# Kernel tuning notes

Measured on AMD Instinct MI355X. Metric: run time of the kernel, lower is better.

The kernel has to match this reference:

```python
import jax, jax.numpy as jnp
import numpy as np

B, N, C, K = 4, 4096, 64, 16
EPS = 1e-5


def _bn(x, g, b, m, v):
    # eval-mode BatchNorm2d on [B, C, N, K]
    scale = (g / jnp.sqrt(v + EPS))[None, :, None, None]
    return (x - m[None, :, None, None]) * scale + b[None, :, None, None]


def setup_inputs() -> dict:
    key = jax.random.key(0)
    ks = jax.random.split(key, 32)
    s = 0.05
    inp = {
        "p": jax.random.normal(ks[0], (B, N, 3), jnp.float32),
        "x": jax.random.normal(ks[1], (B, C, N), jnp.float32),
        "mask": jnp.ones((B, N), dtype=bool),
        # q/k/v 1x1 Conv1d weights [out, in] + bias
        "Wq": jax.random.normal(ks[2], (C, C)) * s, "bq": jax.random.normal(ks[3], (C,)) * s,
        "Wk": jax.random.normal(ks[4], (C, C)) * s, "bk": jax.random.normal(ks[5], (C,)) * s,
        "Wv": jax.random.normal(ks[6], (C, C)) * s, "bv": jax.random.normal(ks[7], (C,)) * s,
        # pos-enc: Conv2d(3->C, no bias), BN, ReLU, Conv2d(C->C)
        "pe_w1": jax.random.normal(ks[8], (C, 3)) * s,
        "pe_bn_g": jax.random.normal(ks[9], (C,)) * s + 1.0,
        "pe_bn_b": jax.random.normal(ks[10], (C,)) * s,
        "pe_bn_m": jax.random.normal(ks[11], (C,)) * s,
        "pe_bn_v": jax.random.uniform(ks[12], (C,), minval=0.5, maxval=1.5),
        "pe_w2": jax.random.normal(ks[13], (C, C)) * s, "pe_b2": jax.random.normal(ks[14], (C,)) * s,
        # attn: BN, ReLU, Conv2d(C->C, no bias), BN, ReLU, Conv2d(C->C)
        "at_bn0_g": jax.random.normal(ks[15], (C,)) * s + 1.0,
        "at_bn0_b": jax.random.normal(ks[16], (C,)) * s,
        "at_bn0_m": jax.random.normal(ks[17], (C,)) * s,
        "at_bn0_v": jax.random.uniform(ks[18], (C,), minval=0.5, maxval=1.5),
        "at_w1": jax.random.normal(ks[19], (C, C)) * s,
        "at_bn1_g": jax.random.normal(ks[20], (C,)) * s + 1.0,
        "at_bn1_b": jax.random.normal(ks[21], (C,)) * s,
        "at_bn1_m": jax.random.normal(ks[22], (C,)) * s,
        "at_bn1_v": jax.random.uniform(ks[23], (C,), minval=0.5, maxval=1.5),
        "at_w2": jax.random.normal(ks[24], (C, C)) * s, "at_b2": jax.random.normal(ks[25], (C,)) * s,
    }
    return inp


def reference(p, x, mask, Wq, bq, Wk, bk, Wv, bv,
              pe_w1, pe_bn_g, pe_bn_b, pe_bn_m, pe_bn_v, pe_w2, pe_b2,
              at_bn0_g, at_bn0_b, at_bn0_m, at_bn0_v, at_w1,
              at_bn1_g, at_bn1_b, at_bn1_m, at_bn1_v, at_w2, at_b2):
    # q, k, v: 1x1 Conv1d -> [B, C, N]
    q = jnp.einsum('oc,bcn->bon', Wq, x) + bq[None, :, None]
    k = jnp.einsum('oc,bcn->bon', Wk, x) + bk[None, :, None]
    v = jnp.einsum('oc,bcn->bon', Wv, x) + bv[None, :, None]

    # ---- knn_point(K, p, p): Euclidean cdist, zero-point masking, topk smallest
    sq = jnp.sum(p * p, axis=-1)                                   # [B, N]
    d2 = sq[:, :, None] + sq[:, None, :] - 2.0 * jnp.einsum('bnc,bmc->bnm', p, p)
    dist = jnp.sqrt(jnp.maximum(d2, 0.0))                          # [B, N, N]
    valid = ~jnp.all(p == 0, axis=-1)                              # [B, N]
    dist = jnp.where(valid[:, None, :], dist, jnp.inf)
    _, idx = jax.lax.top_k(-dist, K)                               # [B, N, K]

    gather = jax.vmap(lambda a, i: a[i])                           # ([N,C],[N,K]) -> [N,K,C]
    n_k = gather(jnp.transpose(k, (0, 2, 1)), idx)                 # [B, N, K, C]
    n_v = gather(jnp.transpose(v, (0, 2, 1)), idx)                 # [B, N, K, C]
    n_p = gather(p, idx)                                           # [B, N, K, 3]

    rel = p[:, :, None, :] - n_p                                   # [B, N, K, 3]
    rel = jnp.transpose(rel, (0, 3, 1, 2))                         # [B, 3, N, K]

    # position encoding MLP
    h = jnp.einsum('oc,bcnk->bonk', pe_w1, rel)
    h = jax.nn.relu(_bn(h, pe_bn_g, pe_bn_b, pe_bn_m, pe_bn_v))
    n_r = jnp.einsum('oc,bcnk->bonk', pe_w2, h) + pe_b2[None, :, None, None]  # [B,C,N,K]

    # attention MLP on (q - n_k + n_r)
    a = q[:, :, :, None] - jnp.transpose(n_k, (0, 3, 1, 2)) + n_r
    a = jax.nn.relu(_bn(a, at_bn0_g, at_bn0_b, at_bn0_m, at_bn0_v))
    a = jnp.einsum('oc,bcnk->bonk', at_w1, a)
    a = jax.nn.relu(_bn(a, at_bn1_g, at_bn1_b, at_bn1_m, at_bn1_v))
    a = jnp.einsum('oc,bcnk->bonk', at_w2, a) + at_b2[None, :, None, None]

    # mask [B,N] broadcast to [B,C,N,K] (masks query rows, as in original)
    a = jnp.where(mask[:, None, :, None], a, -1e10)
    a = jax.nn.softmax(a, axis=-1)
    a = jnp.where(jnp.isnan(a), 0.0, a)

    y = jnp.sum(a * (jnp.transpose(n_v, (0, 3, 1, 2)) + n_r), axis=-1)  # [B, C, N]
    return (p, y)
```

## Files before the change

kernel.cpp:

```cpp
#include <hip/hip_runtime.h>
#include <stdint.h>

#define NB 4
#define NP 4096
#define NC 64
#define NK 16
#define BN_EPS 1e-5f

typedef __attribute__((ext_vector_type(8))) short short8;
typedef __attribute__((ext_vector_type(4))) float f32x4;
typedef unsigned long long u64;

__device__ __forceinline__ short f2bf(float f) {
    unsigned u = __float_as_uint(f);
    unsigned r = (u + 0x7FFFu + ((u >> 16) & 1u)) >> 16;
    return (short)(unsigned short)r;
}

__global__ __launch_bounds__(256) void px_kernel(const float* __restrict__ p,
                                                 float4* __restrict__ px,
                                                 float* __restrict__ pcopy) {
    int gid = blockIdx.x * 256 + threadIdx.x;
    float x = p[gid * 3 + 0], y = p[gid * 3 + 1], z = p[gid * 3 + 2];
    pcopy[gid * 3 + 0] = x; pcopy[gid * 3 + 1] = y; pcopy[gid * 3 + 2] = z;
    float sq = fmaf(z, z, fmaf(y, y, x * x));
    bool inv = (x == 0.0f) && (y == 0.0f) && (z == 0.0f);
    px[gid] = make_float4(x, y, z, inv ? __builtin_inff() : sq);
}

__global__ __launch_bounds__(128) void qkv_kernel(
        const float* __restrict__ x,
        const float* __restrict__ Wq, const float* __restrict__ bq,
        const float* __restrict__ Wk, const float* __restrict__ bk,
        const float* __restrict__ Wv, const float* __restrict__ bv,
        float* __restrict__ outbase) {
    __shared__ float wt[NC * NC];
    __shared__ float bsh[NC];
    const int which = blockIdx.y;
    const float* W    = which == 0 ? Wq : which == 1 ? Wk : Wv;
    const float* bias = which == 0 ? bq : which == 1 ? bk : bv;
    float* out = outbase + (size_t)which * NB * NP * NC;

    for (int e = threadIdx.x; e < NC * NC; e += 128)
        wt[(e & 63) * NC + (e >> 6)] = W[e];
    if (threadIdx.x < NC) bsh[threadIdx.x] = bias[threadIdx.x];
    __syncthreads();

    const int gid = blockIdx.x * 128 + threadIdx.x;
    const int b = gid >> 12, n = gid & (NP - 1);

    float acc[NC];
#pragma unroll
    for (int o = 0; o < NC; ++o) acc[o] = bsh[o];

    const float* xp = x + (size_t)b * NC * NP + n;
    for (int c = 0; c < NC; ++c) {
        float xc = xp[(size_t)c * NP];
        const float4* wr = (const float4*)&wt[c * NC];
#pragma unroll
        for (int o4 = 0; o4 < NC / 4; ++o4) {
            float4 w4 = wr[o4];
            acc[o4 * 4 + 0] = fmaf(w4.x, xc, acc[o4 * 4 + 0]);
            acc[o4 * 4 + 1] = fmaf(w4.y, xc, acc[o4 * 4 + 1]);
            acc[o4 * 4 + 2] = fmaf(w4.z, xc, acc[o4 * 4 + 2]);
            acc[o4 * 4 + 3] = fmaf(w4.w, xc, acc[o4 * 4 + 3]);
        }
    }
    float4* op = (float4*)(out + (size_t)gid * NC);
#pragma unroll
    for (int o4 = 0; o4 < NC / 4; ++o4)
        op[o4] = make_float4(acc[o4 * 4 + 0], acc[o4 * 4 + 1],
                             acc[o4 * 4 + 2], acc[o4 * 4 + 3]);
}

#define KQW 4
#define KCAP 64

__global__ __launch_bounds__(256) void knn_kernel(const float4* __restrict__ px,
                                                  int* __restrict__ idxout) {
    __shared__ float tb[4][KQW * 64];
    __shared__ u64 sbuf[16][KCAP];
    __shared__ int scnt[16];
    const int l = threadIdx.x & 63;
    const int w = threadIdx.x >> 6;
    const int gw = blockIdx.x * 4 + w;
    const int q0 = gw * KQW;
    const int b  = q0 >> 12;
    const float4* pb = px + (size_t)b * NP;

    float4 pn[KQW];
#pragma unroll
    for (int j = 0; j < KQW; ++j) pn[j] = px[q0 + j];
    if (l < KQW) scnt[w * KQW + l] = 0;
    __builtin_amdgcn_wave_barrier();

    float k1[KQW];
#pragma unroll
    for (int j = 0; j < KQW; ++j) k1[j] = __builtin_inff();
#pragma unroll 4
    for (int i = 0; i < NP / 64; ++i) {
        float4 pm = pb[i * 64 + l];
#pragma unroll
        for (int j = 0; j < KQW; ++j) {
            float dot = fmaf(pm.z, pn[j].z, fmaf(pm.y, pn[j].y, pm.x * pn[j].x));
            float d2 = fmaxf((pn[j].w + pm.w) - 2.0f * dot, 0.0f);
            k1[j] = fminf(k1[j], d2);
        }
    }
#pragma unroll
    for (int j = 0; j < KQW; ++j) tb[w][j * 64 + l] = k1[j];
    __builtin_amdgcn_wave_barrier();

    float T[KQW];
#pragma unroll
    for (int j = 0; j < KQW; ++j) {
        const float* tj = &tb[w][j * 64];
        int rank = 0;
#pragma unroll 4
        for (int t = 0; t < 64; t += 4) {
            f32x4 v = *(const f32x4*)&tj[t];
            rank += (v[0] < k1[j]) + (v[1] < k1[j]) + (v[2] < k1[j]) + (v[3] < k1[j]);
        }
        float cand = (rank <= 15) ? k1[j] : -__builtin_inff();
#pragma unroll
        for (int off = 32; off; off >>= 1)
            cand = fmaxf(cand, __shfl_xor(cand, off));
        T[j] = cand;
    }

#pragma unroll 2
    for (int i = 0; i < NP / 64; ++i) {
        int m = i * 64 + l;
        float4 pm = pb[m];
#pragma unroll
        for (int j = 0; j < KQW; ++j) {
            float dot = fmaf(pm.z, pn[j].z, fmaf(pm.y, pn[j].y, pm.x * pn[j].x));
            float d2 = fmaxf((pn[j].w + pm.w) - 2.0f * dot, 0.0f);
            if (d2 <= T[j]) {
                int pos = atomicAdd(&scnt[w * KQW + j], 1);
                if (pos < KCAP)
                    sbuf[w * KQW + j][pos] =
                        ((u64)__float_as_uint(d2) << 32) | (unsigned int)m;
            }
        }
    }
    __builtin_amdgcn_wave_barrier();

#pragma unroll 1
    for (int j = 0; j < KQW; ++j) {
        int cnt = scnt[w * KQW + j];
        if (cnt > KCAP) cnt = KCAP;
        if (l < cnt) {
            const u64* sb = sbuf[w * KQW + j];
            u64 kj = sb[l];
            int rank = 0;
            for (int t = 0; t < cnt; ++t) rank += (sb[t] < kj);
            if (rank < NK)
                idxout[(size_t)(q0 + j) * NK + rank] = (int)(kj & 0xffffffffu);
        }
    }
}

#define QPW 4
#define HBSTR 72
#define DBSTR 20

__device__ __forceinline__ short8 pack8(float4 a, float4 b) {
    short8 r;
    r[0] = f2bf(a.x); r[1] = f2bf(a.y); r[2] = f2bf(a.z); r[3] = f2bf(a.w);
    r[4] = f2bf(b.x); r[5] = f2bf(b.y); r[6] = f2bf(b.z); r[7] = f2bf(b.w);
    return r;
}

__device__ __forceinline__ void gemm_stage(const short8* wf ,
                                           const unsigned short* HBw,
                                           float* DBw, int tok, int quad) {
    short8 b0 = *(const short8*)((const char*)HBw + tok * (HBSTR * 2) + quad * 16);
    short8 b1 = *(const short8*)((const char*)HBw + tok * (HBSTR * 2) + 64 + quad * 16);
#pragma unroll
    for (int ob = 0; ob < 4; ++ob) {
        f32x4 acc = {0.0f, 0.0f, 0.0f, 0.0f};
        acc = __builtin_amdgcn_mfma_f32_16x16x32_bf16(wf[ob * 2 + 0], b0, acc, 0, 0, 0);
        acc = __builtin_amdgcn_mfma_f32_16x16x32_bf16(wf[ob * 2 + 1], b1, acc, 0, 0, 0);
#pragma unroll
        for (int r = 0; r < 4; ++r)
            DBw[(ob * 16 + quad * 4 + r) * DBSTR + tok] = acc[r];
    }
}

__global__ __launch_bounds__(256, 2) void fused_mfma_kernel(
        const float4* __restrict__ px, const int* __restrict__ idx,
        const float* __restrict__ qT, const float* __restrict__ kT,
        const float* __restrict__ vT,
        const float* __restrict__ pe_w1,
        const float* __restrict__ pe_g, const float* __restrict__ pe_b,
        const float* __restrict__ pe_m, const float* __restrict__ pe_v,
        const float* __restrict__ pe_w2, const float* __restrict__ pe_b2,
        const float* __restrict__ b0g, const float* __restrict__ b0b,
        const float* __restrict__ b0m, const float* __restrict__ b0v,
        const float* __restrict__ at_w1,
        const float* __restrict__ b1g, const float* __restrict__ b1b,
        const float* __restrict__ b1m, const float* __restrict__ b1v,
        const float* __restrict__ at_w2, const float* __restrict__ at_b2,
        float* __restrict__ yout) {
    __shared__ __align__(16) unsigned short HB[4][16 * HBSTR];
    __shared__ __align__(16) float DB[4][64 * DBSTR];
    __shared__ __align__(16) int IB[4][NK];

    const int l    = threadIdx.x & 63;
    const int w    = threadIdx.x >> 6;
    const int c    = l;
    const int tok  = l & 15;
    const int quad = l >> 4;

    short8 wf[3][8];
    {
        const float* Ws[3] = {pe_w2, at_w1, at_w2};
#pragma unroll
        for (int mat = 0; mat < 3; ++mat)
#pragma unroll
            for (int ob = 0; ob < 4; ++ob)
#pragma unroll
                for (int ch = 0; ch < 2; ++ch) {
                    const float* src = Ws[mat] + (ob * 16 + tok) * NC + ch * 32 + quad * 8;
                    float4 a = *(const float4*)src;
                    float4 bq4 = *(const float4*)(src + 4);
                    wf[mat][ob * 2 + ch] = pack8(a, bq4);
                }
    }

    const float pw0 = pe_w1[c * 3 + 0], pw1 = pe_w1[c * 3 + 1], pw2v = pe_w1[c * 3 + 2];
    const float pes = pe_g[c] / sqrtf(pe_v[c] + BN_EPS);
    const float peb = fmaf(-pe_m[c], pes, pe_b[c]);
    const float s0  = b0g[c] / sqrtf(b0v[c] + BN_EPS);
    const float bb0 = fmaf(-b0m[c], s0, b0b[c]);
    const float s1  = b1g[c] / sqrtf(b1v[c] + BN_EPS);
    const float bb1 = fmaf(-b1m[c], s1, b1b[c]);
    const float peb2 = pe_b2[c];
    const float ab2  = at_b2[c];

    unsigned short* HBw = HB[w];
    float* DBw = DB[w];
    int* IBw = IB[w];

    const int gw = blockIdx.x * 4 + w;

    for (int jq = 0; jq < QPW; ++jq) {
        const int qi = gw * QPW + jq;
        const int b = qi >> 12, n = qi & (NP - 1);
        const float4 pn = px[qi];
        const float qv = qT[(size_t)qi * NC + c];

        if (l < NK) IBw[l] = idx[qi * NK + l];
        __builtin_amdgcn_wave_barrier();

        int mreg[NK];
#pragma unroll
        for (int g = 0; g < 4; ++g) {
            int4 m4 = *(const int4*)&IBw[g * 4];
            mreg[g * 4 + 0] = m4.x; mreg[g * 4 + 1] = m4.y;
            mreg[g * 4 + 2] = m4.z; mreg[g * 4 + 3] = m4.w;
        }

        float4 pmr[NK];
#pragma unroll
        for (int k = 0; k < NK; ++k) pmr[k] = px[b * NP + mreg[k]];

#pragma unroll
        for (int k = 0; k < NK; ++k) {
            float r0 = pn.x - pmr[k].x, r1 = pn.y - pmr[k].y, r2 = pn.z - pmr[k].z;
            float h = fmaf(pw2v, r2, fmaf(pw1, r1, pw0 * r0));
            h = fmaxf(fmaf(h, pes, peb), 0.0f);
            HBw[k * HBSTR + c] = (unsigned short)f2bf(h);
        }
        __builtin_amdgcn_wave_barrier();

        float kreg[NK];
#pragma unroll
        for (int k = 0; k < NK; ++k)
            kreg[k] = kT[((size_t)(b * NP + mreg[k])) * NC + c];

        gemm_stage(wf[0], HBw, DBw, tok, quad);
        __builtin_amdgcn_wave_barrier();

        float nr[NK];
#pragma unroll
        for (int j = 0; j < 4; ++j) {
            f32x4 v4 = *(const f32x4*)(DBw + c * DBSTR + j * 4);
            nr[j * 4 + 0] = v4[0] + peb2;
            nr[j * 4 + 1] = v4[1] + peb2;
            nr[j * 4 + 2] = v4[2] + peb2;
            nr[j * 4 + 3] = v4[3] + peb2;
        }
        __builtin_amdgcn_wave_barrier();

#pragma unroll
        for (int k = 0; k < NK; ++k) {
            float a0 = qv - kreg[k] + nr[k];
            a0 = fmaxf(fmaf(a0, s0, bb0), 0.0f);
            HBw[k * HBSTR + c] = (unsigned short)f2bf(a0);
        }
        __builtin_amdgcn_wave_barrier();

        float vreg[NK];
#pragma unroll
        for (int k = 0; k < NK; ++k)
            vreg[k] = vT[((size_t)(b * NP + mreg[k])) * NC + c];

        gemm_stage(wf[1], HBw, DBw, tok, quad);
        __builtin_amdgcn_wave_barrier();

#pragma unroll
        for (int j = 0; j < 4; ++j) {
            f32x4 v4 = *(const f32x4*)(DBw + c * DBSTR + j * 4);
#pragma unroll
            for (int r = 0; r < 4; ++r) {
                float a2 = fmaxf(fmaf(v4[r], s1, bb1), 0.0f);
                HBw[(j * 4 + r) * HBSTR + c] = (unsigned short)f2bf(a2);
            }
        }
        __builtin_amdgcn_wave_barrier();

        gemm_stage(wf[2], HBw, DBw, tok, quad);
        __builtin_amdgcn_wave_barrier();

        float a3[NK];
#pragma unroll
        for (int j = 0; j < 4; ++j) {
            f32x4 v4 = *(const f32x4*)(DBw + c * DBSTR + j * 4);
            a3[j * 4 + 0] = v4[0] + ab2;
            a3[j * 4 + 1] = v4[1] + ab2;
            a3[j * 4 + 2] = v4[2] + ab2;
            a3[j * 4 + 3] = v4[3] + ab2;
        }
        __builtin_amdgcn_wave_barrier();

        float mx = a3[0];
#pragma unroll
        for (int k = 1; k < NK; ++k) mx = fmaxf(mx, a3[k]);
        float ssum = 0.0f, yacc = 0.0f;
#pragma unroll
        for (int k = 0; k < NK; ++k) {
            float e = __expf(a3[k] - mx);
            ssum += e;
            yacc = fmaf(e, vreg[k] + nr[k], yacc);
        }
        yout[((size_t)(b * NC + c)) * NP + n] = yacc / ssum;
        __builtin_amdgcn_wave_barrier();
    }
}

extern "C" void kernel_launch(void* const* d_in, const int* in_sizes, int n_in,
                              void* d_out, int out_size, void* d_ws, size_t ws_size,
                              hipStream_t stream) {
    const float* p    = (const float*)d_in[0];
    const float* x    = (const float*)d_in[1];
    const float* Wq = (const float*)d_in[3];  const float* bq = (const float*)d_in[4];
    const float* Wk = (const float*)d_in[5];  const float* bk = (const float*)d_in[6];
    const float* Wv = (const float*)d_in[7];  const float* bv = (const float*)d_in[8];
    const float* pe_w1 = (const float*)d_in[9];
    const float* pe_g  = (const float*)d_in[10]; const float* pe_b = (const float*)d_in[11];
    const float* pe_m  = (const float*)d_in[12]; const float* pe_v = (const float*)d_in[13];
    const float* pe_w2 = (const float*)d_in[14]; const float* pe_b2 = (const float*)d_in[15];
    const float* b0g = (const float*)d_in[16]; const float* b0b = (const float*)d_in[17];
    const float* b0m = (const float*)d_in[18]; const float* b0v = (const float*)d_in[19];
    const float* at_w1 = (const float*)d_in[20];
    const float* b1g = (const float*)d_in[21]; const float* b1b = (const float*)d_in[22];
    const float* b1m = (const float*)d_in[23]; const float* b1v = (const float*)d_in[24];
    const float* at_w2 = (const float*)d_in[25]; const float* at_b2 = (const float*)d_in[26];

    const size_t BNC = (size_t)NB * NP * NC;
    float* ws  = (float*)d_ws;
    float* qT  = ws;
    float* kT  = qT + BNC;
    float* vT  = kT + BNC;
    float4* px = (float4*)(vT + BNC);
    int* idx   = (int*)(px + (size_t)NB * NP);

    float* outp = (float*)d_out;
    float* y = outp + (size_t)NB * NP * 3;

    px_kernel<<<dim3(64), dim3(256), 0, stream>>>(p, px, outp);
    qkv_kernel<<<dim3(128, 3), dim3(128), 0, stream>>>(x, Wq, bq, Wk, bk, Wv, bv, qT);
    knn_kernel<<<dim3(1024), dim3(256), 0, stream>>>(px, idx);
    fused_mfma_kernel<<<dim3(1024), dim3(256), 0, stream>>>(
        px, idx, qT, kT, vT, pe_w1, pe_g, pe_b, pe_m, pe_v, pe_w2, pe_b2,
        b0g, b0b, b0m, b0v, at_w1, b1g, b1b, b1m, b1v, at_w2, at_b2, y);
}
```

Measured before the change: 222.8 us.

## Fold BN scales into weights, merge px into qkv, restructure knn and fused grids

Merges the point-preprocessing kernel into the qkv kernel, which drops one launch. It folds the BatchNorm scales into the q/k weights, the pos-enc first layer and the at_w1 MFMA fragments, removing per-element scaling. knn now handles 8 queries per wave with half the blocks. The fused kernel now runs one query per wave with 4x more blocks and a higher occupancy hint, and keeps fp32 in LDS, converting to bf16 by truncation at fragment load. The truncating conversion changes rounding slightly, and the changed grid shapes shift the balance between occupancy, register pressure and how well weight loads are amortized.

```diff
diff --git a/kernel.cpp b/kernel.cpp
--- a/kernel.cpp
+++ b/kernel.cpp
@@ -17,15 +17,20 @@
     return (short)(unsigned short)r;
 }
 
-__global__ __launch_bounds__(256) void px_kernel(const float* __restrict__ p,
-                                                 float4* __restrict__ px,
-                                                 float* __restrict__ pcopy) {
-    int gid = blockIdx.x * 256 + threadIdx.x;
-    float x = p[gid * 3 + 0], y = p[gid * 3 + 1], z = p[gid * 3 + 2];
-    pcopy[gid * 3 + 0] = x; pcopy[gid * 3 + 1] = y; pcopy[gid * 3 + 2] = z;
-    float sq = fmaf(z, z, fmaf(y, y, x * x));
-    bool inv = (x == 0.0f) && (y == 0.0f) && (z == 0.0f);
-    px[gid] = make_float4(x, y, z, inv ? __builtin_inff() : sq);
+__device__ __forceinline__ short8 packtrunc(f32x4 a, f32x4 b) {
+    union { short8 s; unsigned int w[4]; } r;
+    r.w[0] = __builtin_amdgcn_perm(__float_as_uint(a[1]), __float_as_uint(a[0]), 0x07060302u);
+    r.w[1] = __builtin_amdgcn_perm(__float_as_uint(a[3]), __float_as_uint(a[2]), 0x07060302u);
+    r.w[2] = __builtin_amdgcn_perm(__float_as_uint(b[1]), __float_as_uint(b[0]), 0x07060302u);
+    r.w[3] = __builtin_amdgcn_perm(__float_as_uint(b[3]), __float_as_uint(b[2]), 0x07060302u);
+    return r.s;
+}
+
+__device__ __forceinline__ short8 pack8s(float4 a, float4 b, float s) {
+    short8 r;
+    r[0] = f2bf(a.x * s); r[1] = f2bf(a.y * s); r[2] = f2bf(a.z * s); r[3] = f2bf(a.w * s);
+    r[4] = f2bf(b.x * s); r[5] = f2bf(b.y * s); r[6] = f2bf(b.z * s); r[7] = f2bf(b.w * s);
+    return r;
 }
 
 __global__ __launch_bounds__(128) void qkv_kernel(
@@ -33,20 +38,39 @@
         const float* __restrict__ Wq, const float* __restrict__ bq,
         const float* __restrict__ Wk, const float* __restrict__ bk,
         const float* __restrict__ Wv, const float* __restrict__ bv,
+        const float* __restrict__ b0g, const float* __restrict__ b0v,
+        const float* __restrict__ p, float4* __restrict__ px,
+        float* __restrict__ pcopy,
         float* __restrict__ outbase) {
     __shared__ float wt[NC * NC];
     __shared__ float bsh[NC];
+    __shared__ float sc[NC];
     const int which = blockIdx.y;
     const float* W    = which == 0 ? Wq : which == 1 ? Wk : Wv;
     const float* bias = which == 0 ? bq : which == 1 ? bk : bv;
     float* out = outbase + (size_t)which * NB * NP * NC;
 
+    const int gid = blockIdx.x * 128 + threadIdx.x;
+
+    if (which == 0) {
+        float xx = p[gid * 3 + 0], yy = p[gid * 3 + 1], zz = p[gid * 3 + 2];
+        pcopy[gid * 3 + 0] = xx; pcopy[gid * 3 + 1] = yy; pcopy[gid * 3 + 2] = zz;
+        float sq = fmaf(zz, zz, fmaf(yy, yy, xx * xx));
+        bool inv = (xx == 0.0f) && (yy == 0.0f) && (zz == 0.0f);
+        px[gid] = make_float4(xx, yy, zz, inv ? __builtin_inff() : sq);
+    }
+
+    if (threadIdx.x < NC) {
+        float s = 1.0f;
+        if (which <= 1) s = b0g[threadIdx.x] / sqrtf(b0v[threadIdx.x] + BN_EPS);
+        sc[threadIdx.x] = s;
+        bsh[threadIdx.x] = bias[threadIdx.x] * s;
+    }
+    __syncthreads();
     for (int e = threadIdx.x; e < NC * NC; e += 128)
-        wt[(e & 63) * NC + (e >> 6)] = W[e];
-    if (threadIdx.x < NC) bsh[threadIdx.x] = bias[threadIdx.x];
+        wt[(e & 63) * NC + (e >> 6)] = W[e] * sc[e >> 6];
     __syncthreads();
 
-    const int gid = blockIdx.x * 128 + threadIdx.x;
     const int b = gid >> 12, n = gid & (NP - 1);
 
     float acc[NC];
@@ -73,14 +97,14 @@
                              acc[o4 * 4 + 2], acc[o4 * 4 + 3]);
 }
 
-#define KQW 4
+#define KQW 8
 #define KCAP 64
 
 __global__ __launch_bounds__(256) void knn_kernel(const float4* __restrict__ px,
                                                   int* __restrict__ idxout) {
     __shared__ float tb[4][KQW * 64];
-    __shared__ u64 sbuf[16][KCAP];
-    __shared__ int scnt[16];
+    __shared__ u64 sbuf[4 * KQW][KCAP];
+    __shared__ int scnt[4 * KQW];
     const int l = threadIdx.x & 63;
     const int w = threadIdx.x >> 6;
     const int gw = blockIdx.x * 4 + w;
@@ -112,7 +136,7 @@
     __builtin_amdgcn_wave_barrier();
 
     float T[KQW];
-#pragma unroll
+#pragma unroll 1
     for (int j = 0; j < KQW; ++j) {
         const float* tj = &tb[w][j * 64];
         int rank = 0;
@@ -161,22 +185,19 @@
     }
 }
 
-#define QPW 4
-#define HBSTR 72
+#define HBF 68
 #define DBSTR 20
 
-__device__ __forceinline__ short8 pack8(float4 a, float4 b) {
-    short8 r;
-    r[0] = f2bf(a.x); r[1] = f2bf(a.y); r[2] = f2bf(a.z); r[3] = f2bf(a.w);
-    r[4] = f2bf(b.x); r[5] = f2bf(b.y); r[6] = f2bf(b.z); r[7] = f2bf(b.w);
-    return r;
-}
-
 __device__ __forceinline__ void gemm_stage(const short8* wf ,
-                                           const unsigned short* HBw,
+                                           const float* HBw,
                                            float* DBw, int tok, int quad) {
-    short8 b0 = *(const short8*)((const char*)HBw + tok * (HBSTR * 2) + quad * 16);
-    short8 b1 = *(const short8*)((const char*)HBw + tok * (HBSTR * 2) + 64 + quad * 16);
+    const float* bse = HBw + tok * HBF + quad * 8;
+    f32x4 f0 = *(const f32x4*)(bse);
+    f32x4 f1 = *(const f32x4*)(bse + 4);
+    f32x4 f2 = *(const f32x4*)(bse + 32);
+    f32x4 f3 = *(const f32x4*)(bse + 36);
+    short8 b0 = packtrunc(f0, f1);
+    short8 b1 = packtrunc(f2, f3);
 #pragma unroll
     for (int ob = 0; ob < 4; ++ob) {
         f32x4 acc = {0.0f, 0.0f, 0.0f, 0.0f};
@@ -188,7 +209,7 @@
     }
 }
 
-__global__ __launch_bounds__(256, 2) void fused_mfma_kernel(
+__global__ __launch_bounds__(256, 4) void fused_mfma_kernel(
         const float4* __restrict__ px, const int* __restrict__ idx,
         const float* __restrict__ qT, const float* __restrict__ kT,
         const float* __restrict__ vT,
@@ -203,9 +224,8 @@
         const float* __restrict__ b1m, const float* __restrict__ b1v,
         const float* __restrict__ at_w2, const float* __restrict__ at_b2,
         float* __restrict__ yout) {
-    __shared__ __align__(16) unsigned short HB[4][16 * HBSTR];
+    __shared__ __align__(16) float HB[4][16 * HBF];
     __shared__ __align__(16) float DB[4][64 * DBSTR];
-    __shared__ __align__(16) int IB[4][NK];
 
     const int l    = threadIdx.x & 63;
     const int w    = threadIdx.x >> 6;
@@ -213,141 +233,139 @@
     const int tok  = l & 15;
     const int quad = l >> 4;
 
+    const int qi = blockIdx.x * 4 + w;
+    const int b = qi >> 12, n = qi & (NP - 1);
+
+    int mreg[NK];
+    {
+        const int4* ip = (const int4*)(idx + (size_t)qi * NK);
+#pragma unroll
+        for (int g = 0; g < 4; ++g) {
+            int4 m4 = ip[g];
+            mreg[g * 4 + 0] = m4.x; mreg[g * 4 + 1] = m4.y;
+            mreg[g * 4 + 2] = m4.z; mreg[g * 4 + 3] = m4.w;
+        }
+    }
+    float4 pmr[NK];
+#pragma unroll
+    for (int k = 0; k < NK; ++k) pmr[k] = px[b * NP + mreg[k]];
+    const float4 pn = px[qi];
+    const float qvs = qT[(size_t)qi * NC + c];
+
     short8 wf[3][8];
     {
+        float s1r[4];
+#pragma unroll
+        for (int ob = 0; ob < 4; ++ob) {
+            int m = ob * 16 + tok;
+            s1r[ob] = b1g[m] / sqrtf(b1v[m] + BN_EPS);
+        }
         const float* Ws[3] = {pe_w2, at_w1, at_w2};
 #pragma unroll
         for (int mat = 0; mat < 3; ++mat)
 #pragma unroll
-            for (int ob = 0; ob < 4; ++ob)
+            for (int ob = 0; ob < 4; ++ob) {
+                float fs = (mat == 1) ? s1r[ob] : 1.0f;
 #pragma unroll
                 for (int ch = 0; ch < 2; ++ch) {
                     const float* src = Ws[mat] + (ob * 16 + tok) * NC + ch * 32 + quad * 8;
                     float4 a = *(const float4*)src;
                     float4 bq4 = *(const float4*)(src + 4);
-                    wf[mat][ob * 2 + ch] = pack8(a, bq4);
+                    wf[mat][ob * 2 + ch] = pack8s(a, bq4, fs);
                 }
-    }
-
-    const float pw0 = pe_w1[c * 3 + 0], pw1 = pe_w1[c * 3 + 1], pw2v = pe_w1[c * 3 + 2];
+            }
+    }
+
     const float pes = pe_g[c] / sqrtf(pe_v[c] + BN_EPS);
     const float peb = fmaf(-pe_m[c], pes, pe_b[c]);
-    const float s0  = b0g[c] / sqrtf(b0v[c] + BN_EPS);
-    const float bb0 = fmaf(-b0m[c], s0, b0b[c]);
-    const float s1  = b1g[c] / sqrtf(b1v[c] + BN_EPS);
-    const float bb1 = fmaf(-b1m[c], s1, b1b[c]);
+    const float pw0 = pe_w1[c * 3 + 0] * pes, pw1 = pe_w1[c * 3 + 1] * pes,
+                pw2v = pe_w1[c * 3 + 2] * pes;
+    const float s0c = b0g[c] / sqrtf(b0v[c] + BN_EPS);
+    const float bb0 = fmaf(-b0m[c], s0c, b0b[c]);
+    const float s1c = b1g[c] / sqrtf(b1v[c] + BN_EPS);
+    const float bb1 = fmaf(-b1m[c], s1c, b1b[c]);
     const float peb2 = pe_b2[c];
     const float ab2  = at_b2[c];
 
-    unsigned short* HBw = HB[w];
+    float* HBw = HB[w];
     float* DBw = DB[w];
-    int* IBw = IB[w];
-
-    const int gw = blockIdx.x * 4 + w;
-
-    for (int jq = 0; jq < QPW; ++jq) {
-        const int qi = gw * QPW + jq;
-        const int b = qi >> 12, n = qi & (NP - 1);
-        const float4 pn = px[qi];
-        const float qv = qT[(size_t)qi * NC + c];
-
-        if (l < NK) IBw[l] = idx[qi * NK + l];
-        __builtin_amdgcn_wave_barrier();
-
-        int mreg[NK];
-#pragma unroll
-        for (int g = 0; g < 4; ++g) {
-            int4 m4 = *(const int4*)&IBw[g * 4];
-            mreg[g * 4 + 0] = m4.x; mreg[g * 4 + 1] = m4.y;
-            mreg[g * 4 + 2] = m4.z; mreg[g * 4 + 3] = m4.w;
-        }
-
-        float4 pmr[NK];
-#pragma unroll
-        for (int k = 0; k < NK; ++k) pmr[k] = px[b * NP + mreg[k]];
-
-#pragma unroll
-        for (int k = 0; k < NK; ++k) {
-            float r0 = pn.x - pmr[k].x, r1 = pn.y - pmr[k].y, r2 = pn.z - pmr[k].z;
-            float h = fmaf(pw2v, r2, fmaf(pw1, r1, pw0 * r0));
-            h = fmaxf(fmaf(h, pes, peb), 0.0f);
-            HBw[k * HBSTR + c] = (unsigned short)f2bf(h);
-        }
-        __builtin_amdgcn_wave_barrier();
-
-        float kreg[NK];
-#pragma unroll
-        for (int k = 0; k < NK; ++k)
-            kreg[k] = kT[((size_t)(b * NP + mreg[k])) * NC + c];
-
-        gemm_stage(wf[0], HBw, DBw, tok, quad);
-        __builtin_amdgcn_wave_barrier();
-
-        float nr[NK];
-#pragma unroll
-        for (int j = 0; j < 4; ++j) {
-            f32x4 v4 = *(const f32x4*)(DBw + c * DBSTR + j * 4);
-            nr[j * 4 + 0] = v4[0] + peb2;
-            nr[j * 4 + 1] = v4[1] + peb2;
-            nr[j * 4 + 2] = v4[2] + peb2;
-            nr[j * 4 + 3] = v4[3] + peb2;
-        }
-        __builtin_amdgcn_wave_barrier();
-
-#pragma unroll
-        for (int k = 0; k < NK; ++k) {
-            float a0 = qv - kreg[k] + nr[k];
-            a0 = fmaxf(fmaf(a0, s0, bb0), 0.0f);
-            HBw[k * HBSTR + c] = (unsigned short)f2bf(a0);
-        }
-        __builtin_amdgcn_wave_barrier();
-
-        float vreg[NK];
-#pragma unroll
-        for (int k = 0; k < NK; ++k)
-            vreg[k] = vT[((size_t)(b * NP + mreg[k])) * NC + c];
-
-        gemm_stage(wf[1], HBw, DBw, tok, quad);
-        __builtin_amdgcn_wave_barrier();
-
-#pragma unroll
-        for (int j = 0; j < 4; ++j) {
-            f32x4 v4 = *(const f32x4*)(DBw + c * DBSTR + j * 4);
-#pragma unroll
-            for (int r = 0; r < 4; ++r) {
-                float a2 = fmaxf(fmaf(v4[r], s1, bb1), 0.0f);
-                HBw[(j * 4 + r) * HBSTR + c] = (unsigned short)f2bf(a2);
-            }
-        }
-        __builtin_amdgcn_wave_barrier();
-
-        gemm_stage(wf[2], HBw, DBw, tok, quad);
-        __builtin_amdgcn_wave_barrier();
-
-        float a3[NK];
-#pragma unroll
-        for (int j = 0; j < 4; ++j) {
-            f32x4 v4 = *(const f32x4*)(DBw + c * DBSTR + j * 4);
-            a3[j * 4 + 0] = v4[0] + ab2;
-            a3[j * 4 + 1] = v4[1] + ab2;
-            a3[j * 4 + 2] = v4[2] + ab2;
-            a3[j * 4 + 3] = v4[3] + ab2;
-        }
-        __builtin_amdgcn_wave_barrier();
-
-        float mx = a3[0];
-#pragma unroll
-        for (int k = 1; k < NK; ++k) mx = fmaxf(mx, a3[k]);
-        float ssum = 0.0f, yacc = 0.0f;
-#pragma unroll
-        for (int k = 0; k < NK; ++k) {
-            float e = __expf(a3[k] - mx);
-            ssum += e;
-            yacc = fmaf(e, vreg[k] + nr[k], yacc);
-        }
-        yout[((size_t)(b * NC + c)) * NP + n] = yacc / ssum;
-        __builtin_amdgcn_wave_barrier();
-    }
+
+#pragma unroll
+    for (int k = 0; k < NK; ++k) {
+        float r0 = pn.x - pmr[k].x, r1 = pn.y - pmr[k].y, r2 = pn.z - pmr[k].z;
+        float h = fmaf(pw2v, r2, fmaf(pw1, r1, fmaf(pw0, r0, peb)));
+        HBw[k * HBF + c] = fmaxf(h, 0.0f);
+    }
+    __builtin_amdgcn_wave_barrier();
+
+    float kreg[NK];
+#pragma unroll
+    for (int k = 0; k < NK; ++k)
+        kreg[k] = kT[((size_t)(b * NP + mreg[k])) * NC + c];
+
+    gemm_stage(wf[0], HBw, DBw, tok, quad);
+    __builtin_amdgcn_wave_barrier();
+
+    float nr[NK];
+#pragma unroll
+    for (int j = 0; j < 4; ++j) {
+        f32x4 v4 = *(const f32x4*)(DBw + c * DBSTR + j * 4);
+        nr[j * 4 + 0] = v4[0] + peb2;
+        nr[j * 4 + 1] = v4[1] + peb2;
+        nr[j * 4 + 2] = v4[2] + peb2;
+        nr[j * 4 + 3] = v4[3] + peb2;
+    }
+    __builtin_amdgcn_wave_barrier();
+
+    const float qb = qvs + bb0;
+#pragma unroll
+    for (int k = 0; k < NK; ++k) {
+        float t = qb - kreg[k];
+        HBw[k * HBF + c] = fmaxf(fmaf(s0c, nr[k], t), 0.0f);
+    }
+    __builtin_amdgcn_wave_barrier();
+
+    float vreg[NK];
+#pragma unroll
+    for (int k = 0; k < NK; ++k)
+        vreg[k] = vT[((size_t)(b * NP + mreg[k])) * NC + c];
+
+    gemm_stage(wf[1], HBw, DBw, tok, quad);
+    __builtin_amdgcn_wave_barrier();
+
+#pragma unroll
+    for (int j = 0; j < 4; ++j) {
+        f32x4 v4 = *(const f32x4*)(DBw + c * DBSTR + j * 4);
+#pragma unroll
+        for (int r = 0; r < 4; ++r)
+            HBw[(j * 4 + r) * HBF + c] = fmaxf(v4[r] + bb1, 0.0f);
+    }
+    __builtin_amdgcn_wave_barrier();
+
+    gemm_stage(wf[2], HBw, DBw, tok, quad);
+    __builtin_amdgcn_wave_barrier();
+
+    float a3[NK];
+#pragma unroll
+    for (int j = 0; j < 4; ++j) {
+        f32x4 v4 = *(const f32x4*)(DBw + c * DBSTR + j * 4);
+        a3[j * 4 + 0] = v4[0] + ab2;
+        a3[j * 4 + 1] = v4[1] + ab2;
+        a3[j * 4 + 2] = v4[2] + ab2;
+        a3[j * 4 + 3] = v4[3] + ab2;
+    }
+
+    float mx = a3[0];
+#pragma unroll
+    for (int k = 1; k < NK; ++k) mx = fmaxf(mx, a3[k]);
+    float ssum = 0.0f, yacc = 0.0f;
+#pragma unroll
+    for (int k = 0; k < NK; ++k) {
+        float e = __expf(a3[k] - mx);
+        ssum += e;
+        yacc = fmaf(e, vreg[k] + nr[k], yacc);
+    }
+    yout[((size_t)(b * NC + c)) * NP + n] = yacc / ssum;
 }
 
 extern "C" void kernel_launch(void* const* d_in, const int* in_sizes, int n_in,
@@ -380,10 +398,10 @@
     float* outp = (float*)d_out;
     float* y = outp + (size_t)NB * NP * 3;
 
-    px_kernel<<<dim3(64), dim3(256), 0, stream>>>(p, px, outp);
-    qkv_kernel<<<dim3(128, 3), dim3(128), 0, stream>>>(x, Wq, bq, Wk, bk, Wv, bv, qT);
-    knn_kernel<<<dim3(1024), dim3(256), 0, stream>>>(px, idx);
-    fused_mfma_kernel<<<dim3(1024), dim3(256), 0, stream>>>(
+    qkv_kernel<<<dim3(128, 3), dim3(128), 0, stream>>>(
+        x, Wq, bq, Wk, bk, Wv, bv, b0g, b0v, p, px, outp, qT);
+    knn_kernel<<<dim3(512), dim3(256), 0, stream>>>(px, idx);
+    fused_mfma_kernel<<<dim3(4096), dim3(256), 0, stream>>>(
         px, idx, qT, kT, vT, pe_w1, pe_g, pe_b, pe_m, pe_v, pe_w2, pe_b2,
         b0g, b0b, b0m, b0v, at_w1, b1g, b1b, b1m, b1v, at_w2, at_b2, y);
 }
```

Measured after the change: 548.3 us. +146.1%, slower.
